# Performance work log

Measured on AMD Instinct MI355X. Metric: run time of the kernel, lower is better.

## Reference

```python
import jax, jax.numpy as jnp
import numpy as np

B, S, D = 2, 2048, 1024
H, DH = 16, 64


def setup_inputs() -> dict:
    key = jax.random.key(0)
    ks = jax.random.split(key, 12)
    scale = 1.0 / np.sqrt(D)
    inp = {
        "queries": jax.random.normal(ks[0], (B, S, D), jnp.float32),
        "keys": jax.random.normal(ks[1], (B, S, D), jnp.float32),
        "values": jax.random.normal(ks[2], (B, S, D), jnp.float32),
        # causal mask: True = masked (strict upper triangle), broadcastable to (B*H, S, S)
        "mask": jnp.triu(jnp.ones((1, S, S), dtype=bool), k=1),
        "Wq": jax.random.normal(ks[3], (D, H * DH), jnp.float32) * scale,
        "bq": jnp.zeros((H * DH,), jnp.float32),
        "Wk": jax.random.normal(ks[4], (D, H * DH), jnp.float32) * scale,
        "bk": jnp.zeros((H * DH,), jnp.float32),
        "Wv": jax.random.normal(ks[5], (D, H * DH), jnp.float32) * scale,
        "bv": jnp.zeros((H * DH,), jnp.float32),
        "Wo": jax.random.normal(ks[6], (H * DH, D), jnp.float32) * scale,
        "bo": jnp.zeros((D,), jnp.float32),
    }
    return inp


def _split_heads(x):
    # (B, S, H*DH) -> (B, H, S, DH)
    b, s, _ = x.shape
    return x.reshape(b, s, H, DH).transpose(0, 2, 1, 3)


def reference(queries, keys, values, mask, Wq, bq, Wk, bk, Wv, bv, Wo, bo):
    q = _split_heads(queries @ Wq + bq)   # (B,H,S,DH)
    k = _split_heads(keys @ Wk + bk)
    v = _split_heads(values @ Wv + bv)
    scores = jnp.einsum("bhqd,bhkd->bhqk", q, k) / jnp.sqrt(jnp.float32(DH))
    m = mask[:, None, :, :]  # (1,1,S,S) broadcast over (B,H,S,S)
    scores = jnp.where(m, -jnp.inf, scores)
    attn = jax.nn.softmax(scores, axis=-1)  # dropout p=0.0 -> identity
    ctx = jnp.einsum("bhqk,bhkd->bhqd", attn, v)
    ctx = ctx.transpose(0, 2, 1, 3).reshape(queries.shape[0], S, H * DH)
    return ctx @ Wo + bo
```

## Files before the change

### kernel.cpp

```cpp
#include <hip/hip_runtime.h>
#include <hip/hip_bf16.h>

#define BB 2
#define SS 2048
#define DDIM 1024
#define HH 16
#define DH 64

typedef __attribute__((ext_vector_type(8))) short bf16x8;
typedef __attribute__((ext_vector_type(4))) short s16x4;
typedef __attribute__((ext_vector_type(4))) float f32x4;
typedef __attribute__((ext_vector_type(16))) float f32x16;

__device__ __forceinline__ short f2bf(float f) {
  unsigned u = __builtin_bit_cast(unsigned, f);
  unsigned r = (u + 0x7fffu + ((u >> 16) & 1u)) >> 16;
  return (short)r;
}

__device__ __forceinline__ unsigned cvtpk(float a, float b) {
  unsigned pk;
  asm("v_cvt_pk_bf16_f32 %0, %1, %2" : "=v"(pk) : "v"(a), "v"(b));
  return pk;
}

__device__ __forceinline__ f32x4 mfma16(bf16x8 a, bf16x8 b, f32x4 c) {
  return __builtin_amdgcn_mfma_f32_16x16x32_bf16(a, b, c, 0, 0, 0);
}
__device__ __forceinline__ f32x16 mfma32(bf16x8 a, bf16x8 b, f32x16 c) {
  return __builtin_amdgcn_mfma_f32_32x32x16_bf16(a, b, c, 0, 0, 0);
}

__device__ __forceinline__ void gload16(const short* g, short* l) {
  __builtin_amdgcn_global_load_lds(
      (const __attribute__((address_space(1))) void*)g,
      (__attribute__((address_space(3))) void*)l, 16, 0, 0);
}

struct TW { const float* W; short* Wt; };
struct TW4 { TW t[4]; };

__global__ __launch_bounds__(256) void transw_k(TW4 ts) {
  __shared__ short tile[64][72];
  const TW tw = ts.t[blockIdx.z];
  const int k0 = blockIdx.x * 64, n0 = blockIdx.y * 64;
  const int tr = threadIdx.x >> 4, tc4 = (threadIdx.x & 15) * 4;
  #pragma unroll
  for (int it = 0; it < 4; ++it) {
    int k = k0 + tr + it * 16;
    float4 v = *(const float4*)(tw.W + (size_t)k * 1024 + n0 + tc4);
    tile[tc4 + 0][tr + it * 16] = f2bf(v.x);
    tile[tc4 + 1][tr + it * 16] = f2bf(v.y);
    tile[tc4 + 2][tr + it * 16] = f2bf(v.z);
    tile[tc4 + 3][tr + it * 16] = f2bf(v.w);
  }
  __syncthreads();
  #pragma unroll
  for (int it = 0; it < 4; ++it) {
    int n = n0 + tr + it * 16;
    s16x4 o;
    o[0] = tile[tr + it * 16][tc4 + 0];
    o[1] = tile[tr + it * 16][tc4 + 1];
    o[2] = tile[tr + it * 16][tc4 + 2];
    o[3] = tile[tr + it * 16][tc4 + 3];
    *(s16x4*)(tw.Wt + (size_t)n * 1024 + k0 + tc4) = o;
  }
}

__global__ __launch_bounds__(256) void transv_k(const short* __restrict__ V,
                                                short* __restrict__ Vt) {
  __shared__ short tile[64][72];
  const int b = blockIdx.z, h = blockIdx.y, s0 = blockIdx.x * 64;
  const int tr = threadIdx.x >> 4, tc4 = (threadIdx.x & 15) * 4;
  #pragma unroll
  for (int it = 0; it < 4; ++it) {
    int sl = tr + it * 16;
    s16x4 v = *(const s16x4*)(V + ((size_t)b * SS + s0 + sl) * DDIM + h * DH + tc4);
    tile[tc4 + 0][sl] = v[0];
    tile[tc4 + 1][sl] = v[1];
    tile[tc4 + 2][sl] = v[2];
    tile[tc4 + 3][sl] = v[3];
  }
  __syncthreads();
  #pragma unroll
  for (int it = 0; it < 4; ++it) {
    int dh = tr + it * 16;
    s16x4 o;
    o[0] = tile[dh][tc4 + 0];
    o[1] = tile[dh][tc4 + 1];
    o[2] = tile[dh][tc4 + 2];
    o[3] = tile[dh][tc4 + 3];
    *(s16x4*)(Vt + ((size_t)(b * HH + h) * DH + dh) * SS + s0 + tc4) = o;
  }
}

struct GB { const void* A; const short* Bt; const float* bias; void* C; float scale; };
struct GB3 { GB g[3]; };

template<int A_F32, int OUT_F32>
__global__ __launch_bounds__(256) void gemm_k(GB3 gbs, int M, int N, int K) {
  __shared__ short As[128 * 32];
  __shared__ short Bs[128 * 32];
  const GB gb = gbs.g[blockIdx.z];
  const int tid = threadIdx.x;
  const int lane = tid & 63, wave = tid >> 6;
  const int wr = (wave >> 1) * 64, wc = (wave & 1) * 64;
  const int g = lane >> 4, r = lane & 15;
  const int bm = blockIdx.x * 128, bn = blockIdx.y * 128;
  const int arow = lane >> 2, acol = (lane & 3) * 8;
  f32x4 acc[4][4] = {};

  for (int k0 = 0; k0 < K; k0 += 32) {
    if (A_F32) {
      const float* Af = (const float*)gb.A;
      #pragma unroll
      for (int it = 0; it < 4; ++it) {
        int row = it * 32 + (tid >> 3);
        int kc = (tid & 7) * 4;
        float4 v = *(const float4*)(Af + (size_t)(bm + row) * K + k0 + kc);
        uint2 u2;
        u2.x = cvtpk(v.x, v.y);
        u2.y = cvtpk(v.z, v.w);
        *(uint2*)&As[row * 32 + kc] = u2;
      }
    } else {
      const short* Ab = (const short*)gb.A;
      #pragma unroll
      for (int s = 0; s < 2; ++s) {
        int rowc = wave * 32 + s * 16;
        gload16(Ab + (size_t)(bm + rowc + arow) * K + k0 + acol, &As[rowc * 32]);
      }
    }
    {
      #pragma unroll
      for (int s = 0; s < 2; ++s) {
        int rowc = wave * 32 + s * 16;
        gload16(gb.Bt + (size_t)(bn + rowc + arow) * K + k0 + acol, &Bs[rowc * 32]);
      }
    }
    __syncthreads();
    bf16x8 af[4], bfr[4];
    #pragma unroll
    for (int m = 0; m < 4; ++m) af[m] = *(const bf16x8*)&As[(wr + m * 16 + r) * 32 + g * 8];
    #pragma unroll
    for (int n = 0; n < 4; ++n) bfr[n] = *(const bf16x8*)&Bs[(wc + n * 16 + r) * 32 + g * 8];
    #pragma unroll
    for (int m = 0; m < 4; ++m)
      #pragma unroll
      for (int n = 0; n < 4; ++n)
        acc[m][n] = mfma16(af[m], bfr[n], acc[m][n]);
    __syncthreads();
  }

  #pragma unroll
  for (int m = 0; m < 4; ++m)
    #pragma unroll
    for (int n = 0; n < 4; ++n) {
      int col = bn + wc + n * 16 + r;
      float bv = gb.bias[col];
      #pragma unroll
      for (int i = 0; i < 4; ++i) {
        int row = bm + wr + m * 16 + g * 4 + i;
        float val = (acc[m][n][i] + bv) * gb.scale;
        if (OUT_F32) ((float*)gb.C)[(size_t)row * N + col] = val;
        else         ((short*)gb.C)[(size_t)row * N + col] = f2bf(val);
      }
    }
}

__global__ __launch_bounds__(256) void attn_k(const short* __restrict__ Q,
                                              const short* __restrict__ Km,
                                              const short* __restrict__ Vt,
                                              short* __restrict__ ctx) {
  __shared__ float SO[3][64][64];
  __shared__ float Sl[3][2][64];

  const int tid = threadIdx.x;
  const int lane = tid & 63, w = tid >> 6;
  const int q31 = lane & 31, hi = lane >> 5;

  const int bid = blockIdx.x;
  const int wid = (bid & 7) * 128 + (bid >> 3);
  const int p = wid & 31;
  const int h = (wid >> 5) & 15;
  const int b = wid >> 9;
  const int qlo = p, qhi = 63 - p;
  const int ntLo = qlo + 1, ntHi = qhi + 1;

  bf16x8 qbL[4], qbH[4];
  {
    const short* qL = Q + ((size_t)b * SS + qlo * 32 + q31) * DDIM + h * DH + hi * 8;
    const short* qH = Q + ((size_t)b * SS + qhi * 32 + q31) * DDIM + h * DH + hi * 8;
    #pragma unroll
    for (int c = 0; c < 4; ++c) {
      qbL[c] = *(const bf16x8*)(qL + c * 16);
      qbH[c] = *(const bf16x8*)(qH + c * 16);
    }
  }

  f32x16 OL0 = {}, OL1 = {}, OH0 = {}, OH1 = {};
  float lL = 0.f, lH = 0.f;

  for (int t = w; t < ntHi; t += 4) {
    const int kv0 = t * 32;
    const short* krow = Km + ((size_t)b * SS + kv0 + q31) * DDIM + h * DH + hi * 8;
    bf16x8 ka0 = *(const bf16x8*)(krow);
    bf16x8 ka1 = *(const bf16x8*)(krow + 16);
    bf16x8 ka2 = *(const bf16x8*)(krow + 32);
    bf16x8 ka3 = *(const bf16x8*)(krow + 48);
    const short* vbase = Vt + ((size_t)((b * HH + h) * DH) + q31) * SS + kv0 + hi * 8;
    bf16x8 vb00 = *(const bf16x8*)(vbase);
    bf16x8 vb01 = *(const bf16x8*)(vbase + (size_t)32 * SS);
    bf16x8 vb10 = *(const bf16x8*)(vbase + 16);
    bf16x8 vb11 = *(const bf16x8*)(vbase + 16 + (size_t)32 * SS);

    const bool loAct = (t < ntLo);

    f32x16 stH = {}, stL = {};
    __builtin_amdgcn_s_setprio(1);
    stH = mfma32(ka0, qbH[0], stH);
    if (loAct) stL = mfma32(ka0, qbL[0], stL);
    stH = mfma32(ka1, qbH[1], stH);
    if (loAct) stL = mfma32(ka1, qbL[1], stL);
    stH = mfma32(ka2, qbH[2], stH);
    if (loAct) stL = mfma32(ka2, qbL[2], stL);
    stH = mfma32(ka3, qbH[3], stH);
    if (loAct) stL = mfma32(ka3, qbL[3], stL);
    __builtin_amdgcn_s_setprio(0);

    auto process = [&](const f32x16& st, float& l,
                       f32x16& O0, f32x16& O1, bool diag) {
      float p16[16];
      float sum = 0.f;
      #pragma unroll
      for (int r = 0; r < 16; ++r) {
        float s = st[r];
        if (diag) {
          int crow = (r & 3) + 8 * (r >> 2) + 4 * hi;
          if (crow > q31) s = -1.0e38f;
        }
        p16[r] = exp2f(s);
        sum += p16[r];
      }
      sum += __shfl_xor(sum, 32);
      l += sum;
      unsigned u[8], x[8];
      #pragma unroll
      for (int j = 0; j < 8; ++j) u[j] = cvtpk(p16[2 * j], p16[2 * j + 1]);
      #pragma unroll
      for (int j = 0; j < 8; ++j) x[j] = (unsigned)__shfl_xor((int)u[j], 32);
      uint4 c0, c1;
      c0.x = hi ? x[2] : u[0];  c0.y = hi ? x[3] : u[1];
      c0.z = hi ? u[2] : x[0];  c0.w = hi ? u[3] : x[1];
      c1.x = hi ? x[6] : u[4];  c1.y = hi ? x[7] : u[5];
      c1.z = hi ? u[6] : x[4];  c1.w = hi ? u[7] : x[5];
      bf16x8 pa0 = __builtin_bit_cast(bf16x8, c0);
      bf16x8 pa1 = __builtin_bit_cast(bf16x8, c1);
      __builtin_amdgcn_s_setprio(1);
      O0 = mfma32(pa0, vb00, O0);
      O1 = mfma32(pa0, vb01, O1);
      O0 = mfma32(pa1, vb10, O0);
      O1 = mfma32(pa1, vb11, O1);
      __builtin_amdgcn_s_setprio(0);
    };

    process(stH, lH, OH0, OH1, t == qhi);
    if (loAct) process(stL, lL, OL0, OL1, t == qlo);
  }

  __syncthreads();
  if (w > 0) {
    const int s = w - 1;
    #pragma unroll
    for (int r = 0; r < 16; ++r) {
      SO[s][r][lane] = OL0[r];
      SO[s][16 + r][lane] = OL1[r];
      SO[s][32 + r][lane] = OH0[r];
      SO[s][48 + r][lane] = OH1[r];
    }
    Sl[s][0][lane] = lL;
    Sl[s][1][lane] = lH;
  }
  __syncthreads();
  if (w == 0) {
    #pragma unroll
    for (int st = 0; st < 2; ++st) {
      float l = (st ? lH : lL) + Sl[0][st][lane] + Sl[1][st][lane] + Sl[2][st][lane];
      float linv = 1.f / l;
      const int qr0 = (st ? qhi : qlo) * 32;
      #pragma unroll
      for (int r = 0; r < 16; ++r) {
        int crow = (r & 3) + 8 * (r >> 2) + 4 * hi;
        float cr = __shfl(linv, crow);
        float o0 = (st ? OH0[r] : OL0[r]) + SO[0][st * 32 + r][lane]
                 + SO[1][st * 32 + r][lane] + SO[2][st * 32 + r][lane];
        float o1 = (st ? OH1[r] : OL1[r]) + SO[0][st * 32 + 16 + r][lane]
                 + SO[1][st * 32 + 16 + r][lane] + SO[2][st * 32 + 16 + r][lane];
        size_t base = ((size_t)b * SS + qr0 + crow) * (HH * DH) + h * DH;
        ctx[base + q31] = f2bf(o0 * cr);
        ctx[base + 32 + q31] = f2bf(o1 * cr);
      }
    }
  }
}

extern "C" void kernel_launch(void* const* d_in, const int* in_sizes, int n_in,
                              void* d_out, int out_size, void* d_ws, size_t ws_size,
                              hipStream_t stream) {
  const float* queries = (const float*)d_in[0];
  const float* keys    = (const float*)d_in[1];
  const float* values  = (const float*)d_in[2];
  const float* Wq = (const float*)d_in[4];
  const float* bq = (const float*)d_in[5];
  const float* Wk = (const float*)d_in[6];
  const float* bk = (const float*)d_in[7];
  const float* Wv = (const float*)d_in[8];
  const float* bv = (const float*)d_in[9];
  const float* Wo = (const float*)d_in[10];
  const float* bo = (const float*)d_in[11];

  char* ws = (char*)d_ws;
  short* Qb  = (short*)(ws);
  short* Kb  = (short*)(ws +  8388608);
  short* Vb  = (short*)(ws + 16777216);
  short* Vtr = (short*)(ws + 25165824);
  short* ctx = Vb;
  short* WqT = (short*)(ws + 33554432);
  short* WkT = (short*)(ws + 35651584);
  short* WvT = (short*)(ws + 37748736);
  short* WoT = (short*)(ws + 39845888);

  const int M = BB * SS, N = HH * DH, K = DDIM;

  TW4 tw;
  tw.t[0] = { Wq, WqT };
  tw.t[1] = { Wk, WkT };
  tw.t[2] = { Wv, WvT };
  tw.t[3] = { Wo, WoT };
  hipLaunchKernelGGL(transw_k, dim3(16, 16, 4), dim3(256), 0, stream, tw);

  GB3 g1;
  g1.g[0] = { queries, WqT, bq, (void*)Qb, 0.18033688f };
  g1.g[1] = { keys,    WkT, bk, (void*)Kb, 1.0f };
  g1.g[2] = { values,  WvT, bv, (void*)Vb, 1.0f };
  hipLaunchKernelGGL((gemm_k<1, 0>), dim3(M / 128, N / 128, 3), dim3(256), 0, stream,
                     g1, M, N, K);

  hipLaunchKernelGGL(transv_k, dim3(SS / 64, HH, BB), dim3(256), 0, stream, Vb, Vtr);

  hipLaunchKernelGGL(attn_k, dim3(1024), dim3(256), 0, stream,
                     Qb, Kb, Vtr, ctx);

  GB3 g3;
  g3.g[0] = { ctx, WoT, bo, d_out, 1.0f };
  g3.g[1] = g3.g[0];
  g3.g[2] = g3.g[0];
  hipLaunchKernelGGL((gemm_k<0, 1>), dim3(M / 128, DDIM / 128, 1), dim3(256), 0, stream,
                     g3, M, DDIM, K);
}
```

Before: 146.9 us.

## Pre-convert inputs to bf16, use single-wave double-buffered GEMM, shrink attention merge LDS

A separate kernel now converts the fp32 query, key and value inputs to bf16 into scratch buffers: d_out for Xq and Xk, and the V-transpose buffer for Xv. The GEMMs can then load A directly into LDS asynchronously. The GEMM is replaced by a one-wave 64x64-tile kernel that double-buffers LDS with vmcnt waits and uses no block barriers. The attention epilogue merges partial outputs in four phases over a smaller LDS buffer, which can raise occupancy. In exchange this adds an extra full pass over the inputs, uses smaller tiles with less reuse, and adds more barriers in the merge.

```diff
diff --git a/kernel.cpp b/kernel.cpp
--- a/kernel.cpp
+++ b/kernel.cpp
@@ -35,6 +35,22 @@
   __builtin_amdgcn_global_load_lds(
       (const __attribute__((address_space(1))) void*)g,
       (__attribute__((address_space(3))) void*)l, 16, 0, 0);
+}
+
+struct CV { const float* src; short* dst; };
+struct CV3 { CV c[3]; };
+
+__global__ __launch_bounds__(256) void conv_k(CV3 cs) {
+  const CV cv = cs.c[blockIdx.z];
+  size_t i = ((size_t)blockIdx.x * 256 + threadIdx.x) * 8;
+  float4 v0 = *(const float4*)(cv.src + i);
+  float4 v1 = *(const float4*)(cv.src + i + 4);
+  uint4 o;
+  o.x = cvtpk(v0.x, v0.y);
+  o.y = cvtpk(v0.z, v0.w);
+  o.z = cvtpk(v1.x, v1.y);
+  o.w = cvtpk(v1.z, v1.w);
+  *(uint4*)(cv.dst + i) = o;
 }
 
 struct TW { const float* W; short* Wt; };
@@ -97,70 +113,58 @@
 struct GB { const void* A; const short* Bt; const float* bias; void* C; float scale; };
 struct GB3 { GB g[3]; };
 
-template<int A_F32, int OUT_F32>
-__global__ __launch_bounds__(256) void gemm_k(GB3 gbs, int M, int N, int K) {
-  __shared__ short As[128 * 32];
-  __shared__ short Bs[128 * 32];
+template<int OUT_F32>
+__global__ __launch_bounds__(64) void gemm1w_k(GB3 gbs, int M, int N, int K) {
+  __shared__ short As[2][64 * 32];
+  __shared__ short Bs[2][64 * 32];
   const GB gb = gbs.g[blockIdx.z];
-  const int tid = threadIdx.x;
-  const int lane = tid & 63, wave = tid >> 6;
-  const int wr = (wave >> 1) * 64, wc = (wave & 1) * 64;
-  const int g = lane >> 4, r = lane & 15;
-  const int bm = blockIdx.x * 128, bn = blockIdx.y * 128;
+  const int lane = threadIdx.x;
+  const int r = lane & 15, g = lane >> 4;
   const int arow = lane >> 2, acol = (lane & 3) * 8;
+  const int bm = blockIdx.x * 64, bn = blockIdx.y * 64;
+  const short* Ab = (const short*)gb.A;
+  const short* Bt = gb.Bt;
   f32x4 acc[4][4] = {};
 
-  for (int k0 = 0; k0 < K; k0 += 32) {
-    if (A_F32) {
-      const float* Af = (const float*)gb.A;
-      #pragma unroll
-      for (int it = 0; it < 4; ++it) {
-        int row = it * 32 + (tid >> 3);
-        int kc = (tid & 7) * 4;
-        float4 v = *(const float4*)(Af + (size_t)(bm + row) * K + k0 + kc);
-        uint2 u2;
-        u2.x = cvtpk(v.x, v.y);
-        u2.y = cvtpk(v.z, v.w);
-        *(uint2*)&As[row * 32 + kc] = u2;
-      }
+  auto stage = [&](int buf, int k0) {
+    #pragma unroll
+    for (int s = 0; s < 4; ++s) {
+      gload16(Ab + (size_t)(bm + s * 16 + arow) * K + k0 + acol, &As[buf][s * 16 * 32]);
+      gload16(Bt + (size_t)(bn + s * 16 + arow) * K + k0 + acol, &Bs[buf][s * 16 * 32]);
+    }
+  };
+
+  stage(0, 0);
+  const int nk = K / 32;
+  for (int ks = 0; ks < nk; ++ks) {
+    const int cur = ks & 1;
+    if (ks + 1 < nk) {
+      stage(cur ^ 1, (ks + 1) * 32);
+      asm volatile("s_waitcnt vmcnt(8)" ::: "memory");
     } else {
-      const short* Ab = (const short*)gb.A;
-      #pragma unroll
-      for (int s = 0; s < 2; ++s) {
-        int rowc = wave * 32 + s * 16;
-        gload16(Ab + (size_t)(bm + rowc + arow) * K + k0 + acol, &As[rowc * 32]);
-      }
-    }
-    {
-      #pragma unroll
-      for (int s = 0; s < 2; ++s) {
-        int rowc = wave * 32 + s * 16;
-        gload16(gb.Bt + (size_t)(bn + rowc + arow) * K + k0 + acol, &Bs[rowc * 32]);
-      }
-    }
-    __syncthreads();
+      asm volatile("s_waitcnt vmcnt(0)" ::: "memory");
+    }
     bf16x8 af[4], bfr[4];
     #pragma unroll
-    for (int m = 0; m < 4; ++m) af[m] = *(const bf16x8*)&As[(wr + m * 16 + r) * 32 + g * 8];
-    #pragma unroll
-    for (int n = 0; n < 4; ++n) bfr[n] = *(const bf16x8*)&Bs[(wc + n * 16 + r) * 32 + g * 8];
+    for (int m = 0; m < 4; ++m) af[m] = *(const bf16x8*)&As[cur][(m * 16 + r) * 32 + g * 8];
+    #pragma unroll
+    for (int n = 0; n < 4; ++n) bfr[n] = *(const bf16x8*)&Bs[cur][(n * 16 + r) * 32 + g * 8];
     #pragma unroll
     for (int m = 0; m < 4; ++m)
       #pragma unroll
       for (int n = 0; n < 4; ++n)
         acc[m][n] = mfma16(af[m], bfr[n], acc[m][n]);
-    __syncthreads();
   }
 
   #pragma unroll
   for (int m = 0; m < 4; ++m)
     #pragma unroll
     for (int n = 0; n < 4; ++n) {
-      int col = bn + wc + n * 16 + r;
+      int col = bn + n * 16 + r;
       float bv = gb.bias[col];
       #pragma unroll
       for (int i = 0; i < 4; ++i) {
-        int row = bm + wr + m * 16 + g * 4 + i;
+        int row = bm + m * 16 + g * 4 + i;
         float val = (acc[m][n][i] + bv) * gb.scale;
         if (OUT_F32) ((float*)gb.C)[(size_t)row * N + col] = val;
         else         ((short*)gb.C)[(size_t)row * N + col] = f2bf(val);
@@ -172,7 +176,7 @@
                                               const short* __restrict__ Km,
                                               const short* __restrict__ Vt,
                                               short* __restrict__ ctx) {
-  __shared__ float SO[3][64][64];
+  __shared__ float SO[3][16][64];
   __shared__ float Sl[3][2][64];
 
   const int tid = threadIdx.x;
@@ -233,14 +237,14 @@
       float p16[16];
       float sum = 0.f;
       #pragma unroll
-      for (int r = 0; r < 16; ++r) {
-        float s = st[r];
+      for (int r2 = 0; r2 < 16; ++r2) {
+        float s = st[r2];
         if (diag) {
-          int crow = (r & 3) + 8 * (r >> 2) + 4 * hi;
+          int crow = (r2 & 3) + 8 * (r2 >> 2) + 4 * hi;
           if (crow > q31) s = -1.0e38f;
         }
-        p16[r] = exp2f(s);
-        sum += p16[r];
+        p16[r2] = exp2f(s);
+        sum += p16[r2];
       }
       sum += __shfl_xor(sum, 32);
       l += sum;
@@ -268,20 +272,28 @@
     if (loAct) process(stL, lL, OL0, OL1, t == qlo);
   }
 
+  if (w > 0) {
+    Sl[w - 1][0][lane] = lL;
+    Sl[w - 1][1][lane] = lH;
+  }
+#define MERGE_PHASE(OV)                                                        \
+  if (w > 0) {                                                                 \
+    _Pragma("unroll") for (int r2 = 0; r2 < 16; ++r2)                          \
+        SO[w - 1][r2][lane] = OV[r2];                                          \
+  }                                                                            \
+  __syncthreads();                                                             \
+  if (w == 0) {                                                                \
+    _Pragma("unroll") for (int r2 = 0; r2 < 16; ++r2)                          \
+        OV[r2] += SO[0][r2][lane] + SO[1][r2][lane] + SO[2][r2][lane];         \
+  }                                                                            \
   __syncthreads();
-  if (w > 0) {
-    const int s = w - 1;
-    #pragma unroll
-    for (int r = 0; r < 16; ++r) {
-      SO[s][r][lane] = OL0[r];
-      SO[s][16 + r][lane] = OL1[r];
-      SO[s][32 + r][lane] = OH0[r];
-      SO[s][48 + r][lane] = OH1[r];
-    }
-    Sl[s][0][lane] = lL;
-    Sl[s][1][lane] = lH;
-  }
-  __syncthreads();
+
+  MERGE_PHASE(OL0)
+  MERGE_PHASE(OL1)
+  MERGE_PHASE(OH0)
+  MERGE_PHASE(OH1)
+#undef MERGE_PHASE
+
   if (w == 0) {
     #pragma unroll
     for (int st = 0; st < 2; ++st) {
@@ -289,13 +301,11 @@
       float linv = 1.f / l;
       const int qr0 = (st ? qhi : qlo) * 32;
       #pragma unroll
-      for (int r = 0; r < 16; ++r) {
-        int crow = (r & 3) + 8 * (r >> 2) + 4 * hi;
+      for (int r2 = 0; r2 < 16; ++r2) {
+        int crow = (r2 & 3) + 8 * (r2 >> 2) + 4 * hi;
         float cr = __shfl(linv, crow);
-        float o0 = (st ? OH0[r] : OL0[r]) + SO[0][st * 32 + r][lane]
-                 + SO[1][st * 32 + r][lane] + SO[2][st * 32 + r][lane];
-        float o1 = (st ? OH1[r] : OL1[r]) + SO[0][st * 32 + 16 + r][lane]
-                 + SO[1][st * 32 + 16 + r][lane] + SO[2][st * 32 + 16 + r][lane];
+        float o0 = st ? OH0[r2] : OL0[r2];
+        float o1 = st ? OH1[r2] : OL1[r2];
         size_t base = ((size_t)b * SS + qr0 + crow) * (HH * DH) + h * DH;
         ctx[base + q31] = f2bf(o0 * cr);
         ctx[base + 32 + q31] = f2bf(o1 * cr);
@@ -330,6 +340,10 @@
   short* WvT = (short*)(ws + 37748736);
   short* WoT = (short*)(ws + 39845888);
 
+  short* Xq = (short*)d_out;
+  short* Xk = (short*)d_out + 4194304;
+  short* Xv = Vtr;
+
   const int M = BB * SS, N = HH * DH, K = DDIM;
 
   TW4 tw;
@@ -339,11 +353,17 @@
   tw.t[3] = { Wo, WoT };
   hipLaunchKernelGGL(transw_k, dim3(16, 16, 4), dim3(256), 0, stream, tw);
 
+  CV3 cv;
+  cv.c[0] = { queries, Xq };
+  cv.c[1] = { keys,    Xk };
+  cv.c[2] = { values,  Xv };
+  hipLaunchKernelGGL(conv_k, dim3(2048, 1, 3), dim3(256), 0, stream, cv);
+
   GB3 g1;
-  g1.g[0] = { queries, WqT, bq, (void*)Qb, 0.18033688f };
-  g1.g[1] = { keys,    WkT, bk, (void*)Kb, 1.0f };
-  g1.g[2] = { values,  WvT, bv, (void*)Vb, 1.0f };
-  hipLaunchKernelGGL((gemm_k<1, 0>), dim3(M / 128, N / 128, 3), dim3(256), 0, stream,
+  g1.g[0] = { Xq, WqT, bq, (void*)Qb, 0.18033688f };
+  g1.g[1] = { Xk, WkT, bk, (void*)Kb, 1.0f };
+  g1.g[2] = { Xv, WvT, bv, (void*)Vb, 1.0f };
+  hipLaunchKernelGGL((gemm1w_k<0>), dim3(M / 64, N / 64, 3), dim3(64), 0, stream,
                      g1, M, N, K);
 
   hipLaunchKernelGGL(transv_k, dim3(SS / 64, HH, BB), dim3(256), 0, stream, Vb, Vtr);
@@ -355,6 +375,6 @@
   g3.g[0] = { ctx, WoT, bo, d_out, 1.0f };
   g3.g[1] = g3.g[0];
   g3.g[2] = g3.g[0];
-  hipLaunchKernelGGL((gemm_k<0, 1>), dim3(M / 128, DDIM / 128, 1), dim3(256), 0, stream,
+  hipLaunchKernelGGL((gemm1w_k<1>), dim3(M / 64, DDIM / 64, 1), dim3(64), 0, stream,
                      g3, M, DDIM, K);
 }
```

Result: slower. 164.3 us (+11.9%).
